# Optimization experiments

Hardware: AMD Instinct MI355X
Metric: run time of the kernel (lower is better)

The kernel has to match this reference:

```python
import jax, jax.numpy as jnp
import numpy as np

N = 50000      # num_nodes
E = 400000     # num_edges
ND = 128       # node_dim (== hidden_dim of GraphNetwork)
HID = 128      # per-head hidden dim in GAT layer
HEADS = 4      # GAT default num_heads
L = 3          # num_layers


def setup_inputs() -> dict:
    key = jax.random.key(0)
    ks = jax.random.split(key, 12)
    s = lambda k, shape, fan: (jax.random.normal(k, shape, jnp.float32) / np.sqrt(fan)).astype(jnp.float32)
    return dict(
        node_features=jax.random.normal(ks[0], (N, ND), jnp.float32),
        edge_index=jax.random.randint(ks[1], (2, E), 0, N, dtype=jnp.int32),
        enc_w1=s(ks[2], (ND, HID), ND), enc_b1=jnp.zeros((HID,), jnp.float32),
        enc_w2=s(ks[3], (HID, HID), HID), enc_b2=jnp.zeros((HID,), jnp.float32),
        gat_W=s(ks[4], (L, HID, HEADS * HID), HID),
        gat_a_src=s(ks[5], (L, HEADS, HID), HID),
        gat_a_dst=s(ks[6], (L, HEADS, HID), HID),
        gat_out_w=s(ks[7], (L, HEADS * HID, HID), HEADS * HID),
        gat_out_b=jnp.zeros((L, HID), jnp.float32),
        out_w1=s(ks[8], (HID, HID), HID), out_b1=jnp.zeros((HID,), jnp.float32),
        out_w2=s(ks[9], (HID, HID), HID), out_b2=jnp.zeros((HID,), jnp.float32),
    )


def _gat_layer(x, row, col, W, a_src, a_dst, ow, ob):
    """One GraphAttentionLayer (eval mode: dropout disabled)."""
    n = x.shape[0]
    h = (x @ W).reshape(n, HEADS, HID)                       # [N,H,D]
    # per-node attention logits (equivalent to (h[row]*a_src).sum(-1) gathered)
    s_src = jnp.einsum('nhd,hd->nh', h, a_src)               # [N,H]
    s_dst = jnp.einsum('nhd,hd->nh', h, a_dst)               # [N,H]
    e = s_src[row] + s_dst[col]                              # [E,H]
    e = jnp.where(e > 0, e, 0.2 * e)                         # LeakyReLU(0.2)
    e_exp = jnp.exp(e)                                       # matches torch: raw exp, no max-shift
    e_sum = jax.ops.segment_sum(e_exp, col, num_segments=n)  # [N,H]
    alpha = e_exp / (e_sum[col] + 1e-8)                      # [E,H]
    msg = h[row] * alpha[:, :, None]                         # [E,H,D]
    out = jax.ops.segment_sum(msg, col, num_segments=n)      # [N,H,D]
    out = out.reshape(n, HEADS * HID) @ ow + ob              # out_proj
    return x + out                                           # residual


def reference(node_features, edge_index, enc_w1, enc_b1, enc_w2, enc_b2,
              gat_W, gat_a_src, gat_a_dst, gat_out_w, gat_out_b,
              out_w1, out_b1, out_w2, out_b2):
    row, col = edge_index[0], edge_index[1]
    # node encoder: Linear-ReLU-Linear
    h = jax.nn.relu(node_features @ enc_w1 + enc_b1) @ enc_w2 + enc_b2
    for i in range(L):
        h = _gat_layer(h, row, col, gat_W[i], gat_a_src[i], gat_a_dst[i],
                       gat_out_w[i], gat_out_b[i])
    # output MLP: Linear-ReLU-Linear
    h = jax.nn.relu(h @ out_w1 + out_b1) @ out_w2 + out_b2
    # batch is None, global_pooling='mean'
    graph_embedding = h.mean(axis=0, keepdims=True)          # [1,HID]
    return h, graph_embedding
```

## Files before the change

### kernel.cpp

```cpp
#include <hip/hip_runtime.h>
#include <math.h>

typedef unsigned short ushort_t;
typedef __attribute__((ext_vector_type(8))) unsigned short ushortx8;
typedef __attribute__((ext_vector_type(4))) unsigned short ushortx4;
typedef __attribute__((ext_vector_type(4))) float floatx4;
typedef __attribute__((ext_vector_type(8))) short frag8;

__device__ __forceinline__ float bf2f(ushort_t u){
  union {unsigned int i; float f;} v; v.i = ((unsigned int)u)<<16; return v.f;
}
__device__ __forceinline__ ushort_t f2bf(float f){
  union {float f; unsigned int i;} v; v.f = f;
  unsigned int x = v.i;
  unsigned int r = x + 0x7fffu + ((x>>16)&1u);
  return (ushort_t)(r>>16);
}

__device__ __forceinline__ void gload16(const void* g, void* l){
  __builtin_amdgcn_global_load_lds(
      (const __attribute__((address_space(1))) unsigned int*)g,
      (__attribute__((address_space(3))) unsigned int*)l, 16, 0, 0);
}

__global__ __launch_bounds__(256) void k_count(const int* __restrict__ col, int* __restrict__ cnt, int E){
  int e = blockIdx.x*256 + threadIdx.x;
  if (e < E) atomicAdd(&cnt[col[e]], 1);
}

__global__ __launch_bounds__(256) void k_scan1(const int* __restrict__ cnt, int* __restrict__ offs,
                                               int* __restrict__ partials, int n){
  __shared__ int buf[256];
  int tid = threadIdx.x;
  int gid = blockIdx.x*256 + tid;
  int v = (gid < n) ? cnt[gid] : 0;
  buf[tid] = v; __syncthreads();
  #pragma unroll
  for (int off=1; off<256; off<<=1){
    int t = (tid >= off) ? buf[tid-off] : 0;
    __syncthreads();
    buf[tid] += t;
    __syncthreads();
  }
  if (gid < n) offs[gid] = buf[tid] - v;
  if (tid == 255) partials[blockIdx.x] = buf[255];
}

__global__ __launch_bounds__(256) void k_scan2(int* __restrict__ partials, int nb){
  __shared__ int buf[256];
  int tid = threadIdx.x;
  int v = (tid < nb) ? partials[tid] : 0;
  buf[tid] = v; __syncthreads();
  #pragma unroll
  for (int off=1; off<256; off<<=1){
    int t = (tid >= off) ? buf[tid-off] : 0;
    __syncthreads();
    buf[tid] += t;
    __syncthreads();
  }
  partials[tid] = buf[tid] - v;
}

__global__ __launch_bounds__(256) void k_scan3(int* __restrict__ offs, const int* __restrict__ partials,
                                               int n, int E){
  int gid = blockIdx.x*256 + threadIdx.x;
  if (gid < n) offs[gid] += partials[blockIdx.x];
  if (blockIdx.x == 0 && threadIdx.x == 0) offs[n] = E;
}

__global__ __launch_bounds__(256) void k_fill(const int* __restrict__ row, const int* __restrict__ col,
                                              const int* __restrict__ offs, int* __restrict__ fill,
                                              int* __restrict__ rowS, int E){
  int e = blockIdx.x*256 + threadIdx.x;
  if (e >= E) return;
  int c = col[e];
  int pos = offs[c] + atomicAdd(&fill[c], 1);
  rowS[pos] = row[e];
}

template<int K, int NC, int CNT>
__global__ __launch_bounds__(256) void k_convT_b(const float* __restrict__ src, ushort_t* __restrict__ dst){
  int idx = blockIdx.x*256 + threadIdx.x;
  if (idx >= CNT*K*NC) return;
  int l = idx / (K*NC);
  int rem = idx - l*(K*NC);
  int k = rem / NC, n = rem - k*NC;
  dst[(size_t)l*K*NC + (size_t)n*K + k] = f2bf(src[idx]);
}

__global__ __launch_bounds__(256) void k_convT4(const float* __restrict__ s0, const float* __restrict__ s1,
                                                const float* __restrict__ s2, const float* __restrict__ s3,
                                                ushort_t* __restrict__ d0, ushort_t* __restrict__ d1,
                                                ushort_t* __restrict__ d2, ushort_t* __restrict__ d3){
  int idx = blockIdx.x*256 + threadIdx.x;
  if (idx >= 4*16384) return;
  int which = idx >> 14;
  int rem = idx & 16383;
  int k = rem >> 7, n = rem & 127;
  const float* s = which==0 ? s0 : which==1 ? s1 : which==2 ? s2 : s3;
  ushort_t*    d = which==0 ? d0 : which==1 ? d1 : which==2 ? d2 : d3;
  d[n*128 + k] = f2bf(s[rem]);
}

__device__ __forceinline__ void stage_tile64(const ushort_t* src, int ld, int row0, int M, int kc,
                                             ushort_t* lds, int tid){
  int wid = tid>>6, lane = tid&63;
  #pragma unroll
  for (int i=0;i<4;i++){
    int chunk = wid*256 + i*64 + lane;
    int r = chunk>>3, c8 = chunk&7;
    int gr = row0 + r; if (gr >= M) gr = M-1;
    gload16(src + (size_t)gr*ld + kc + c8*8, (char*)lds + (size_t)chunk*16);
  }
}
__device__ __forceinline__ void stage_w128(const ushort_t* src, ushort_t* lds, int tid){
  #pragma unroll
  for (int i=0;i<8;i++){
    int chunk = tid + 256*i;
    gload16(src + (size_t)chunk*8, (char*)lds + (size_t)chunk*16);
  }
}

template<int SA,int SB,int NKS>
__device__ __forceinline__ void ldsgemm(const ushort_t* LA, const ushort_t* LB,
                                        floatx4 (&acc)[4][4], int wr,int wc,int lm,int lk){
  #pragma unroll
  for (int ks=0; ks<NKS; ks++){
    frag8 a[4], b[4];
    #pragma unroll
    for (int mi=0;mi<4;mi++) a[mi] = *(const frag8*)&LA[(wr+mi*16+lm)*SA + ks*32 + lk];
    #pragma unroll
    for (int ni=0;ni<4;ni++) b[ni] = *(const frag8*)&LB[(wc+ni*16+lm)*SB + ks*32 + lk];
    #pragma unroll
    for (int mi=0;mi<4;mi++)
      #pragma unroll
      for (int ni=0;ni<4;ni++)
        acc[mi][ni] = __builtin_amdgcn_mfma_f32_16x16x32_bf16(a[mi], b[ni], acc[mi][ni], 0, 0, 0);
  }
}

__device__ __forceinline__ void zero_acc(floatx4 (&acc)[4][4]){
  #pragma unroll
  for (int i=0;i<4;i++)
    #pragma unroll
    for (int j=0;j<4;j++) acc[i][j] = floatx4{0.f,0.f,0.f,0.f};
}

__device__ __forceinline__ void sdst_block(const floatx4 (&acc)[4][4],
    const float* avec_s, const float* avec_d, float* s_src, float* s_dst, float* sred,
    int head, int bm, int M, int tid, int wid, int lane, int wr, int wc, int lm, int lr4){
  float avs[4], avd[4];
  #pragma unroll
  for (int ni=0;ni<4;ni++){
    int d = wc + ni*16 + lm;
    avs[ni] = avec_s[head*128 + d];
    avd[ni] = avec_d[head*128 + d];
  }
  float pss[4][4], psd[4][4];
  #pragma unroll
  for (int mi=0;mi<4;mi++){
    #pragma unroll
    for (int r=0;r<4;r++){
      float vs = 0.f, vd = 0.f;
      #pragma unroll
      for (int ni=0;ni<4;ni++){
        float v = acc[mi][ni][r];
        vs += v * avs[ni];
        vd += v * avd[ni];
      }
      #pragma unroll
      for (int m=1;m<16;m<<=1){
        vs += __shfl_xor(vs, m);
        vd += __shfl_xor(vd, m);
      }
      pss[mi][r] = vs; psd[mi][r] = vd;
    }
  }
  if (lm == 0){
    #pragma unroll
    for (int mi=0;mi<4;mi++)
      #pragma unroll
      for (int r=0;r<4;r++){
        int rl = wr + mi*16 + lr4 + r;
        sred[0*256 + (wid&1)*128 + rl] = pss[mi][r];
        sred[1*256 + (wid&1)*128 + rl] = psd[mi][r];
      }
  }
  __syncthreads();
  int sd = tid >> 7, rl = tid & 127;
  float v = sred[sd*256 + rl] + sred[sd*256 + 128 + rl];
  int rowg = bm + rl;
  if (rowg < M) (sd ? s_dst : s_src)[(size_t)rowg*4 + head] = v;
}

__device__ __forceinline__ void wgemm_heads(const ushort_t* LA_xb, ushort_t* LB,
    const ushort_t* WT, const float* avs, const float* avd,
    ushort_t* h, float* s_src, float* s_dst, float* sred,
    int bm, int M, int tid, int wid, int lane, int wr, int wc, int lm, int lk, int lr4){
  for (int hb=0; hb<4; hb++){
    __syncthreads();
    stage_w128(WT + (size_t)hb*16384, LB, tid);
    __syncthreads();
    floatx4 acc[4][4]; zero_acc(acc);
    ldsgemm<128,128,4>(LA_xb, LB, acc, wr, wc, lm, lk);
    #pragma unroll
    for (int mi=0;mi<4;mi++){
      #pragma unroll
      for (int ni=0;ni<4;ni++){
        int colg = wc + ni*16 + lm;
        #pragma unroll
        for (int r=0;r<4;r++){
          int rowg = bm + wr + mi*16 + lr4 + r;
          if (rowg < M) h[(size_t)rowg*512 + hb*128 + colg] = f2bf(acc[mi][ni][r]);
        }
      }
    }
    sdst_block(acc, avs, avd, s_src, s_dst, sred, hb, bm, M, tid, wid, lane, wr, wc, lm, lr4);
  }
}

__global__ __launch_bounds__(256) void k_enc(
    const float* __restrict__ nodef,
    const ushort_t* __restrict__ e1T, const float* __restrict__ eb1,
    const ushort_t* __restrict__ e2T, const float* __restrict__ eb2,
    const ushort_t* __restrict__ WT, const float* __restrict__ avs, const float* __restrict__ avd,
    float* __restrict__ x, ushort_t* __restrict__ h,
    float* __restrict__ s_src, float* __restrict__ s_dst, int M)
{
  __shared__ ushort_t LA[128*128];
  __shared__ ushort_t LB[128*128];
  __shared__ float sred[512];
  const int tid = threadIdx.x, wid = tid>>6, lane = tid&63;
  const int bm = blockIdx.x*128;
  const int wr = (wid>>1)*64, wc = (wid&1)*64, lm = lane&15, lk = (lane>>4)*8, lr4 = (lane>>4)*4;

  #pragma unroll
  for (int i=0;i<8;i++){
    int chunk = tid + 256*i;
    int r = chunk>>4, c8 = chunk&15;
    int gr = bm + r; if (gr >= M) gr = M-1;
    floatx4 lo = *(const floatx4*)(nodef + (size_t)gr*128 + c8*8);
    floatx4 hi = *(const floatx4*)(nodef + (size_t)gr*128 + c8*8 + 4);
    ushortx8 v;
    #pragma unroll
    for (int j=0;j<4;j++){ v[j] = f2bf(lo[j]); v[j+4] = f2bf(hi[j]); }
    *(ushortx8*)&LA[r*128 + c8*8] = v;
  }
  stage_w128(e1T, LB, tid);
  __syncthreads();

  floatx4 acc[4][4]; zero_acc(acc);
  ldsgemm<128,128,4>(LA, LB, acc, wr, wc, lm, lk);
  __syncthreads();
  #pragma unroll
  for (int mi=0;mi<4;mi++)
    #pragma unroll
    for (int ni=0;ni<4;ni++){
      int cl = wc + ni*16 + lm;
      float b = eb1[cl];
      #pragma unroll
      for (int r=0;r<4;r++){
        float v = acc[mi][ni][r] + b;
        v = v > 0.f ? v : 0.f;
        LA[(wr + mi*16 + lr4 + r)*128 + cl] = f2bf(v);
      }
    }
  stage_w128(e2T, LB, tid);
  __syncthreads();

  zero_acc(acc);
  ldsgemm<128,128,4>(LA, LB, acc, wr, wc, lm, lk);
  __syncthreads();
  #pragma unroll
  for (int mi=0;mi<4;mi++)
    #pragma unroll
    for (int ni=0;ni<4;ni++){
      int cl = wc + ni*16 + lm;
      float b = eb2[cl];
      #pragma unroll
      for (int r=0;r<4;r++){
        int rl = wr + mi*16 + lr4 + r;
        int rowg = bm + rl;
        float v = acc[mi][ni][r] + b;
        if (rowg < M) x[(size_t)rowg*128 + cl] = v;
        LA[rl*128 + cl] = f2bf(v);
      }
    }

  wgemm_heads(LA, LB, WT, avs, avd, h, s_src, s_dst, sred,
              bm, M, tid, wid, lane, wr, wc, lm, lk, lr4);
}

__global__ __launch_bounds__(256) void k_mid(
    const ushort_t* __restrict__ msg, const ushort_t* __restrict__ OT, const float* __restrict__ ob,
    const ushort_t* __restrict__ WT, const float* __restrict__ avs, const float* __restrict__ avd,
    float* __restrict__ x, ushort_t* __restrict__ h,
    float* __restrict__ s_src, float* __restrict__ s_dst, int M)
{
  __shared__ ushort_t LA[128*128];
  __shared__ ushort_t LB[128*128];
  __shared__ float sred[512];
  const int tid = threadIdx.x, wid = tid>>6, lane = tid&63;
  const int bm = blockIdx.x*128;
  const int wr = (wid>>1)*64, wc = (wid&1)*64, lm = lane&15, lk = (lane>>4)*8, lr4 = (lane>>4)*4;

  floatx4 acc[4][4]; zero_acc(acc);
  for (int kc = 0; kc < 512; kc += 64){
    stage_tile64(msg, 512, bm, M, kc, LA, tid);
    stage_tile64(OT,  512, 0, 128, kc, LB, tid);
    __syncthreads();
    ldsgemm<64,64,2>(LA, LB, acc, wr, wc, lm, lk);
    __syncthreads();
  }
  #pragma unroll
  for (int mi=0;mi<4;mi++)
    #pragma unroll
    for (int ni=0;ni<4;ni++){
      int cl = wc + ni*16 + lm;
      float b = ob[cl];
      #pragma unroll
      for (int r=0;r<4;r++){
        int rl = wr + mi*16 + lr4 + r;
        int rowg = bm + rl;
        float v = acc[mi][ni][r] + b;
        if (rowg < M){
          v += x[(size_t)rowg*128 + cl];
          x[(size_t)rowg*128 + cl] = v;
        }
        LA[rl*128 + cl] = f2bf(v);
      }
    }

  wgemm_heads(LA, LB, WT, avs, avd, h, s_src, s_dst, sred,
              bm, M, tid, wid, lane, wr, wc, lm, lk, lr4);
}

__global__ __launch_bounds__(256) void k_tail(
    const ushort_t* __restrict__ msg, const ushort_t* __restrict__ OT, const float* __restrict__ ob,
    const ushort_t* __restrict__ m1T, const float* __restrict__ mb1,
    const ushort_t* __restrict__ m2T, const float* __restrict__ mb2,
    const float* __restrict__ x, float* __restrict__ out, float* __restrict__ cpart, int M)
{
  __shared__ ushort_t LA[128*128];
  __shared__ ushort_t LB[128*128];
  __shared__ float sredc[256];
  const int tid = threadIdx.x, wid = tid>>6, lane = tid&63;
  const int bm = blockIdx.x*128;
  const int wr = (wid>>1)*64, wc = (wid&1)*64, lm = lane&15, lk = (lane>>4)*8, lr4 = (lane>>4)*4;

  floatx4 acc[4][4]; zero_acc(acc);
  for (int kc = 0; kc < 512; kc += 64){
    stage_tile64(msg, 512, bm, M, kc, LA, tid);
    stage_tile64(OT,  512, 0, 128, kc, LB, tid);
    __syncthreads();
    ldsgemm<64,64,2>(LA, LB, acc, wr, wc, lm, lk);
    __syncthreads();
  }
  #pragma unroll
  for (int mi=0;mi<4;mi++)
    #pragma unroll
    for (int ni=0;ni<4;ni++){
      int cl = wc + ni*16 + lm;
      float b = ob[cl];
      #pragma unroll
      for (int r=0;r<4;r++){
        int rl = wr + mi*16 + lr4 + r;
        int rowg = bm + rl;
        float v = acc[mi][ni][r] + b;
        if (rowg < M) v += x[(size_t)rowg*128 + cl];
        LA[rl*128 + cl] = f2bf(v);
      }
    }
  stage_w128(m1T, LB, tid);
  __syncthreads();

  zero_acc(acc);
  ldsgemm<128,128,4>(LA, LB, acc, wr, wc, lm, lk);
  __syncthreads();
  #pragma unroll
  for (int mi=0;mi<4;mi++)
    #pragma unroll
    for (int ni=0;ni<4;ni++){
      int cl = wc + ni*16 + lm;
      float b = mb1[cl];
      #pragma unroll
      for (int r=0;r<4;r++){
        float v = acc[mi][ni][r] + b;
        v = v > 0.f ? v : 0.f;
        LA[(wr + mi*16 + lr4 + r)*128 + cl] = f2bf(v);
      }
    }
  stage_w128(m2T, LB, tid);
  __syncthreads();

  zero_acc(acc);
  ldsgemm<128,128,4>(LA, LB, acc, wr, wc, lm, lk);

  float csum[4];
  #pragma unroll
  for (int i=0;i<4;i++) csum[i] = 0.f;
  #pragma unroll
  for (int mi=0;mi<4;mi++)
    #pragma unroll
    for (int ni=0;ni<4;ni++){
      int cl = wc + ni*16 + lm;
      float b = mb2[cl];
      #pragma unroll
      for (int r=0;r<4;r++){
        int rowg = bm + wr + mi*16 + lr4 + r;
        if (rowg < M){
          float v = acc[mi][ni][r] + b;
          out[(size_t)rowg*128 + cl] = v;
          csum[ni] += v;
        }
      }
    }
  __syncthreads();
  #pragma unroll
  for (int ni=0;ni<4;ni++){
    float cs = csum[ni];
    cs += __shfl_xor(cs, 16);
    cs += __shfl_xor(cs, 32);
    if (lane < 16) sredc[(wid>>1)*128 + wc + ni*16 + lane] = cs;
  }
  __syncthreads();
  if (tid < 128) cpart[(size_t)blockIdx.x*128 + tid] = sredc[tid] + sredc[128 + tid];
}

__global__ __launch_bounds__(256) void k_gather(const ushort_t* __restrict__ h,
    const float* __restrict__ s_src, const float* __restrict__ s_dst,
    const int* __restrict__ offs, const int* __restrict__ rowS,
    ushort_t* __restrict__ msg, int N)
{
  int wid = threadIdx.x >> 6, lane = threadIdx.x & 63;
  int n = blockIdx.x*4 + wid;
  if (n >= N) return;
  int beg = offs[n], end = offs[n+1];
  const int sub  = lane & 15;
  const int head = lane >> 4;
  const float sdv = s_dst[(size_t)n*4 + head];
  const int c0 = lane*8;

  float acc[8];
  #pragma unroll
  for (int k=0;k<8;k++) acc[k] = 0.f;
  float dsum = 0.f;

  for (int chunk = beg; chunk < end; chunk += 16){
    int m = end - chunk; if (m > 16) m = 16;
    int q = chunk + (sub < m ? sub : m-1);
    int r_p = rowS[q];
    float ss = s_src[(size_t)r_p*4 + head];
    float e = ss + sdv;
    e = e > 0.f ? e : 0.2f*e;
    float w = __expf(e);
    if (sub >= m) w = 0.f;
    dsum += w;

    int j = 0;
    for (; j+1 < m; j += 2){
      int r0 = __shfl(r_p, j);
      int r1 = __shfl(r_p, j+1);
      float w0 = __shfl(w, head*16 + j);
      float w1 = __shfl(w, head*16 + j+1);
      ushortx8 h0 = *(const ushortx8*)(h + (size_t)r0*512 + c0);
      ushortx8 h1 = *(const ushortx8*)(h + (size_t)r1*512 + c0);
      #pragma unroll
      for (int k=0;k<8;k++) acc[k] += w0 * bf2f(h0[k]);
      #pragma unroll
      for (int k=0;k<8;k++) acc[k] += w1 * bf2f(h1[k]);
    }
    if (j < m){
      int r0 = __shfl(r_p, j);
      float w0 = __shfl(w, head*16 + j);
      ushortx8 h0 = *(const ushortx8*)(h + (size_t)r0*512 + c0);
      #pragma unroll
      for (int k=0;k<8;k++) acc[k] += w0 * bf2f(h0[k]);
    }
  }

  float d = dsum;
  #pragma unroll
  for (int mask=1; mask<16; mask<<=1) d += __shfl_xor(d, mask);
  float invd = 1.0f / (d + 1e-8f);

  ushortx8 o;
  #pragma unroll
  for (int k=0;k<8;k++) o[k] = f2bf(acc[k]*invd);
  *(ushortx8*)(msg + (size_t)n*512 + c0) = o;
}

__global__ __launch_bounds__(256) void k_csum2(const float* __restrict__ part, float* __restrict__ out,
                                               int nb, int N){
  __shared__ float buf[256];
  int c = threadIdx.x & 127, half = threadIdx.x >> 7;
  float s = 0.f;
  for (int b = half; b < nb; b += 2) s += part[(size_t)b*128 + c];
  buf[threadIdx.x] = s; __syncthreads();
  if (threadIdx.x < 128) out[c] = (buf[c] + buf[128 + c]) / (float)N;
}

extern "C" void kernel_launch(void* const* d_in, const int* in_sizes, int n_in,
                              void* d_out, int out_size, void* d_ws, size_t ws_size,
                              hipStream_t stream)
{
  const int N = in_sizes[0] / 128;
  const int E = in_sizes[1] / 2;

  const float* nodef  = (const float*)d_in[0];
  const int*   row    = (const int*)d_in[1];
  const int*   col    = row + E;
  const float* enc_w1 = (const float*)d_in[2];
  const float* enc_b1 = (const float*)d_in[3];
  const float* enc_w2 = (const float*)d_in[4];
  const float* enc_b2 = (const float*)d_in[5];
  const float* gat_W  = (const float*)d_in[6];
  const float* a_src  = (const float*)d_in[7];
  const float* a_dst  = (const float*)d_in[8];
  const float* out_w  = (const float*)d_in[9];
  const float* out_b  = (const float*)d_in[10];
  const float* w1     = (const float*)d_in[11];
  const float* b1     = (const float*)d_in[12];
  const float* w2     = (const float*)d_in[13];
  const float* b2     = (const float*)d_in[14];

  char* p = (char*)d_ws;
  auto alloc = [&](size_t bytes)->char*{
    char* r = p; p += (bytes + 255) & ~(size_t)255; return r;
  };
  float*    x     = (float*)   alloc((size_t)N*128*4);
  ushort_t* msg   = (ushort_t*)alloc((size_t)N*512*2);
  ushort_t* h     = (ushort_t*)alloc((size_t)N*512*2);
  float*    s_src = (float*)   alloc((size_t)N*4*4);
  float*    s_dst = (float*)   alloc((size_t)N*4*4);
  int*      offs  = (int*)     alloc(((size_t)N+1)*4);
  int*      rowS  = (int*)     alloc((size_t)E*4);
  int*      cnt   = (int*)     alloc((size_t)N*4);
  int*      fill  = (int*)     alloc((size_t)N*4);
  int*      parts = (int*)     alloc(1024);
  float*    cpart = (float*)   alloc((size_t)((N+127)/128)*128*4);
  ushort_t* wt_e1 = (ushort_t*)alloc(16384*2);
  ushort_t* wt_e2 = (ushort_t*)alloc(16384*2);
  ushort_t* wt_W  = (ushort_t*)alloc((size_t)3*65536*2);
  ushort_t* wt_o  = (ushort_t*)alloc((size_t)3*65536*2);
  ushort_t* wt_m1 = (ushort_t*)alloc(16384*2);
  ushort_t* wt_m2 = (ushort_t*)alloc(16384*2);

  hipMemsetAsync(cnt, 0, (size_t)N*4, stream);
  hipMemsetAsync(fill, 0, (size_t)N*4, stream);

  const int gE = (E + 255)/256;
  const int gN = (N + 255)/256;
  const int gW = (N + 3)/4;
  const int gy = (N + 127)/128;
  dim3 blk(256);

  k_count<<<gE, blk, 0, stream>>>(col, cnt, E);
  k_scan1<<<gN, blk, 0, stream>>>(cnt, offs, parts, N);
  k_scan2<<<1,  blk, 0, stream>>>(parts, gN);
  k_scan3<<<gN, blk, 0, stream>>>(offs, parts, N, E);
  k_fill <<<gE, blk, 0, stream>>>(row, col, offs, fill, rowS, E);

  k_convT4<<<(4*16384+255)/256, blk, 0, stream>>>(enc_w1, enc_w2, w1, w2, wt_e1, wt_e2, wt_m1, wt_m2);
  k_convT_b<128,512,3><<<(3*65536+255)/256, blk, 0, stream>>>(gat_W, wt_W);
  k_convT_b<512,128,3><<<(3*65536+255)/256, blk, 0, stream>>>(out_w, wt_o);

  k_enc<<<gy, blk, 0, stream>>>(nodef, wt_e1, enc_b1, wt_e2, enc_b2,
                                wt_W, a_src, a_dst, x, h, s_src, s_dst, N);

  for (int l = 0; l < 3; l++){
    k_gather<<<gW, blk, 0, stream>>>(h, s_src, s_dst, offs, rowS, msg, N);
    if (l < 2){
      k_mid<<<gy, blk, 0, stream>>>(msg, wt_o + (size_t)l*65536, out_b + (size_t)l*128,
                                    wt_W + (size_t)(l+1)*65536,
                                    a_src + (size_t)(l+1)*512, a_dst + (size_t)(l+1)*512,
                                    x, h, s_src, s_dst, N);
    } else {
      k_tail<<<gy, blk, 0, stream>>>(msg, wt_o + (size_t)2*65536, out_b + (size_t)2*128,
                                     wt_m1, b1, wt_m2, b2,
                                     x, (float*)d_out, cpart, N);
    }
  }
  k_csum2<<<1, blk, 0, stream>>>(cpart, (float*)d_out + (size_t)N*128, gy, N);
}
```

Measured before the change: 538.6 us.

## Read GEMM B fragments from global memory, swizzle A tile in LDS, raise occupancy

The GEMM kernels stop staging weight matrices into LDS and read the B fragments directly from global memory, which is expected to be served from cache. The A tile in LDS now uses an XOR swizzle to avoid bank conflicts, and the K loop over msg stages 128-wide tiles. Halving LDS per block allows launch_bounds(256,3), giving three blocks per CU. The aggregation kernel also writes msg with nontemporal stores. The cost is that B loads from global memory have higher latency and the register budget is tighter.

```diff
diff --git a/kernel.cpp b/kernel.cpp
--- a/kernel.cpp
+++ b/kernel.cpp
@@ -102,35 +102,42 @@
   d[n*128 + k] = f2bf(s[rem]);
 }
 
-__device__ __forceinline__ void stage_tile64(const ushort_t* src, int ld, int row0, int M, int kc,
-                                             ushort_t* lds, int tid){
-  int wid = tid>>6, lane = tid&63;
-  #pragma unroll
-  for (int i=0;i<4;i++){
-    int chunk = wid*256 + i*64 + lane;
-    int r = chunk>>3, c8 = chunk&7;
-    int gr = row0 + r; if (gr >= M) gr = M-1;
-    gload16(src + (size_t)gr*ld + kc + c8*8, (char*)lds + (size_t)chunk*16);
-  }
-}
-__device__ __forceinline__ void stage_w128(const ushort_t* src, ushort_t* lds, int tid){
+
+__device__ __forceinline__ void la_store(ushort_t* LA, int row, int col, ushort_t v){
+  LA[row*128 + ((((col>>3) ^ (row&7))<<3) | (col&7))] = v;
+}
+__device__ __forceinline__ void la_store8(ushort_t* LA, int row, int cg, ushortx8 v){
+  *(ushortx8*)&LA[row*128 + ((cg ^ (row&7))<<3)] = v;
+}
+
+__device__ __forceinline__ void stage_tile128_swz(const ushort_t* src, int ld, int row0, int M, int kc,
+                                                  ushort_t* lds, int tid){
   #pragma unroll
   for (int i=0;i<8;i++){
     int chunk = tid + 256*i;
-    gload16(src + (size_t)chunk*8, (char*)lds + (size_t)chunk*16);
-  }
-}
-
-template<int SA,int SB,int NKS>
-__device__ __forceinline__ void ldsgemm(const ushort_t* LA, const ushort_t* LB,
-                                        floatx4 (&acc)[4][4], int wr,int wc,int lm,int lk){
+    int r = chunk>>4, cg = chunk&15;
+    int gr = row0 + r; if (gr >= M) gr = M-1;
+    int scg = cg ^ (r&7);
+    gload16(src + (size_t)gr*ld + kc + scg*8, (char*)lds + (size_t)chunk*16);
+  }
+}
+
+template<int NKS>
+__device__ __forceinline__ void gemm_swzA_gB(const ushort_t* LA, const ushort_t* __restrict__ BT, int ldb,
+                                             floatx4 (&acc)[4][4], int wr,int wc,int lm,int lk){
   #pragma unroll
   for (int ks=0; ks<NKS; ks++){
-    frag8 a[4], b[4];
-    #pragma unroll
-    for (int mi=0;mi<4;mi++) a[mi] = *(const frag8*)&LA[(wr+mi*16+lm)*SA + ks*32 + lk];
-    #pragma unroll
-    for (int ni=0;ni<4;ni++) b[ni] = *(const frag8*)&LB[(wc+ni*16+lm)*SB + ks*32 + lk];
+    frag8 b[4];
+    #pragma unroll
+    for (int ni=0;ni<4;ni++)
+      b[ni] = *(const frag8*)&BT[(size_t)(wc+ni*16+lm)*ldb + ks*32 + lk];
+    frag8 a[4];
+    int cg = ks*4 + (lk>>3);
+    #pragma unroll
+    for (int mi=0;mi<4;mi++){
+      int row = wr + mi*16 + lm;
+      a[mi] = *(const frag8*)&LA[row*128 + ((cg ^ (row&7))<<3)];
+    }
     #pragma unroll
     for (int mi=0;mi<4;mi++)
       #pragma unroll
@@ -193,16 +200,14 @@
   if (rowg < M) (sd ? s_dst : s_src)[(size_t)rowg*4 + head] = v;
 }
 
-__device__ __forceinline__ void wgemm_heads(const ushort_t* LA_xb, ushort_t* LB,
-    const ushort_t* WT, const float* avs, const float* avd,
+__device__ __forceinline__ void wgemm_heads(const ushort_t* LA,
+    const ushort_t* __restrict__ WT, const float* avs, const float* avd,
     ushort_t* h, float* s_src, float* s_dst, float* sred,
     int bm, int M, int tid, int wid, int lane, int wr, int wc, int lm, int lk, int lr4){
   for (int hb=0; hb<4; hb++){
     __syncthreads();
-    stage_w128(WT + (size_t)hb*16384, LB, tid);
-    __syncthreads();
     floatx4 acc[4][4]; zero_acc(acc);
-    ldsgemm<128,128,4>(LA_xb, LB, acc, wr, wc, lm, lk);
+    gemm_swzA_gB<4>(LA, WT + (size_t)hb*16384, 128, acc, wr, wc, lm, lk);
     #pragma unroll
     for (int mi=0;mi<4;mi++){
       #pragma unroll
@@ -219,7 +224,7 @@
   }
 }
 
-__global__ __launch_bounds__(256) void k_enc(
+__global__ __launch_bounds__(256,3) void k_enc(
     const float* __restrict__ nodef,
     const ushort_t* __restrict__ e1T, const float* __restrict__ eb1,
     const ushort_t* __restrict__ e2T, const float* __restrict__ eb2,
@@ -228,7 +233,6 @@
     float* __restrict__ s_src, float* __restrict__ s_dst, int M)
 {
   __shared__ ushort_t LA[128*128];
-  __shared__ ushort_t LB[128*128];
   __shared__ float sred[512];
   const int tid = threadIdx.x, wid = tid>>6, lane = tid&63;
   const int bm = blockIdx.x*128;
@@ -237,20 +241,19 @@
   #pragma unroll
   for (int i=0;i<8;i++){
     int chunk = tid + 256*i;
-    int r = chunk>>4, c8 = chunk&15;
+    int r = chunk>>4, cg = chunk&15;
     int gr = bm + r; if (gr >= M) gr = M-1;
-    floatx4 lo = *(const floatx4*)(nodef + (size_t)gr*128 + c8*8);
-    floatx4 hi = *(const floatx4*)(nodef + (size_t)gr*128 + c8*8 + 4);
+    floatx4 lo = *(const floatx4*)(nodef + (size_t)gr*128 + cg*8);
+    floatx4 hi = *(const floatx4*)(nodef + (size_t)gr*128 + cg*8 + 4);
     ushortx8 v;
     #pragma unroll
     for (int j=0;j<4;j++){ v[j] = f2bf(lo[j]); v[j+4] = f2bf(hi[j]); }
-    *(ushortx8*)&LA[r*128 + c8*8] = v;
-  }
-  stage_w128(e1T, LB, tid);
+    la_store8(LA, r, cg, v);
+  }
   __syncthreads();
 
   floatx4 acc[4][4]; zero_acc(acc);
-  ldsgemm<128,128,4>(LA, LB, acc, wr, wc, lm, lk);
+  gemm_swzA_gB<4>(LA, e1T, 128, acc, wr, wc, lm, lk);
   __syncthreads();
   #pragma unroll
   for (int mi=0;mi<4;mi++)
@@ -262,14 +265,13 @@
       for (int r=0;r<4;r++){
         float v = acc[mi][ni][r] + b;
         v = v > 0.f ? v : 0.f;
-        LA[(wr + mi*16 + lr4 + r)*128 + cl] = f2bf(v);
-      }
-    }
-  stage_w128(e2T, LB, tid);
+        la_store(LA, wr + mi*16 + lr4 + r, cl, f2bf(v));
+      }
+    }
   __syncthreads();
 
   zero_acc(acc);
-  ldsgemm<128,128,4>(LA, LB, acc, wr, wc, lm, lk);
+  gemm_swzA_gB<4>(LA, e2T, 128, acc, wr, wc, lm, lk);
   __syncthreads();
   #pragma unroll
   for (int mi=0;mi<4;mi++)
@@ -283,33 +285,31 @@
         int rowg = bm + rl;
         float v = acc[mi][ni][r] + b;
         if (rowg < M) x[(size_t)rowg*128 + cl] = v;
-        LA[rl*128 + cl] = f2bf(v);
-      }
-    }
-
-  wgemm_heads(LA, LB, WT, avs, avd, h, s_src, s_dst, sred,
+        la_store(LA, rl, cl, f2bf(v));
+      }
+    }
+
+  wgemm_heads(LA, WT, avs, avd, h, s_src, s_dst, sred,
               bm, M, tid, wid, lane, wr, wc, lm, lk, lr4);
 }
 
-__global__ __launch_bounds__(256) void k_mid(
+__global__ __launch_bounds__(256,3) void k_mid(
     const ushort_t* __restrict__ msg, const ushort_t* __restrict__ OT, const float* __restrict__ ob,
     const ushort_t* __restrict__ WT, const float* __restrict__ avs, const float* __restrict__ avd,
     float* __restrict__ x, ushort_t* __restrict__ h,
     float* __restrict__ s_src, float* __restrict__ s_dst, int M)
 {
   __shared__ ushort_t LA[128*128];
-  __shared__ ushort_t LB[128*128];
   __shared__ float sred[512];
   const int tid = threadIdx.x, wid = tid>>6, lane = tid&63;
   const int bm = blockIdx.x*128;
   const int wr = (wid>>1)*64, wc = (wid&1)*64, lm = lane&15, lk = (lane>>4)*8, lr4 = (lane>>4)*4;
 
   floatx4 acc[4][4]; zero_acc(acc);
-  for (int kc = 0; kc < 512; kc += 64){
-    stage_tile64(msg, 512, bm, M, kc, LA, tid);
-    stage_tile64(OT,  512, 0, 128, kc, LB, tid);
-    __syncthreads();
-    ldsgemm<64,64,2>(LA, LB, acc, wr, wc, lm, lk);
+  for (int kc = 0; kc < 512; kc += 128){
+    stage_tile128_swz(msg, 512, bm, M, kc, LA, tid);
+    __syncthreads();
+    gemm_swzA_gB<4>(LA, OT + kc, 512, acc, wr, wc, lm, lk);
     __syncthreads();
   }
   #pragma unroll
@@ -327,33 +327,31 @@
           v += x[(size_t)rowg*128 + cl];
           x[(size_t)rowg*128 + cl] = v;
         }
-        LA[rl*128 + cl] = f2bf(v);
-      }
-    }
-
-  wgemm_heads(LA, LB, WT, avs, avd, h, s_src, s_dst, sred,
+        la_store(LA, rl, cl, f2bf(v));
+      }
+    }
+
+  wgemm_heads(LA, WT, avs, avd, h, s_src, s_dst, sred,
               bm, M, tid, wid, lane, wr, wc, lm, lk, lr4);
 }
 
-__global__ __launch_bounds__(256) void k_tail(
+__global__ __launch_bounds__(256,3) void k_tail(
     const ushort_t* __restrict__ msg, const ushort_t* __restrict__ OT, const float* __restrict__ ob,
     const ushort_t* __restrict__ m1T, const float* __restrict__ mb1,
     const ushort_t* __restrict__ m2T, const float* __restrict__ mb2,
     const float* __restrict__ x, float* __restrict__ out, float* __restrict__ cpart, int M)
 {
   __shared__ ushort_t LA[128*128];
-  __shared__ ushort_t LB[128*128];
   __shared__ float sredc[256];
   const int tid = threadIdx.x, wid = tid>>6, lane = tid&63;
   const int bm = blockIdx.x*128;
   const int wr = (wid>>1)*64, wc = (wid&1)*64, lm = lane&15, lk = (lane>>4)*8, lr4 = (lane>>4)*4;
 
   floatx4 acc[4][4]; zero_acc(acc);
-  for (int kc = 0; kc < 512; kc += 64){
-    stage_tile64(msg, 512, bm, M, kc, LA, tid);
-    stage_tile64(OT,  512, 0, 128, kc, LB, tid);
-    __syncthreads();
-    ldsgemm<64,64,2>(LA, LB, acc, wr, wc, lm, lk);
+  for (int kc = 0; kc < 512; kc += 128){
+    stage_tile128_swz(msg, 512, bm, M, kc, LA, tid);
+    __syncthreads();
+    gemm_swzA_gB<4>(LA, OT + kc, 512, acc, wr, wc, lm, lk);
     __syncthreads();
   }
   #pragma unroll
@@ -368,14 +366,13 @@
         int rowg = bm + rl;
         float v = acc[mi][ni][r] + b;
         if (rowg < M) v += x[(size_t)rowg*128 + cl];
-        LA[rl*128 + cl] = f2bf(v);
-      }
-    }
-  stage_w128(m1T, LB, tid);
+        la_store(LA, rl, cl, f2bf(v));
+      }
+    }
   __syncthreads();
 
   zero_acc(acc);
-  ldsgemm<128,128,4>(LA, LB, acc, wr, wc, lm, lk);
+  gemm_swzA_gB<4>(LA, m1T, 128, acc, wr, wc, lm, lk);
   __syncthreads();
   #pragma unroll
   for (int mi=0;mi<4;mi++)
@@ -387,14 +384,13 @@
       for (int r=0;r<4;r++){
         float v = acc[mi][ni][r] + b;
         v = v > 0.f ? v : 0.f;
-        LA[(wr + mi*16 + lr4 + r)*128 + cl] = f2bf(v);
-      }
-    }
-  stage_w128(m2T, LB, tid);
+        la_store(LA, wr + mi*16 + lr4 + r, cl, f2bf(v));
+      }
+    }
   __syncthreads();
 
   zero_acc(acc);
-  ldsgemm<128,128,4>(LA, LB, acc, wr, wc, lm, lk);
+  gemm_swzA_gB<4>(LA, m2T, 128, acc, wr, wc, lm, lk);
 
   float csum[4];
   #pragma unroll
@@ -487,7 +483,7 @@
   ushortx8 o;
   #pragma unroll
   for (int k=0;k<8;k++) o[k] = f2bf(acc[k]*invd);
-  *(ushortx8*)(msg + (size_t)n*512 + c0) = o;
+  __builtin_nontemporal_store(o, (ushortx8*)(msg + (size_t)n*512 + c0));
 }
 
 __global__ __launch_bounds__(256) void k_csum2(const float* __restrict__ part, float* __restrict__ out,
```

Measured after the change: 567.4 us. 1.05x slower.
